# Performance work log

Hardware: AMD Instinct MI355X
Metric: run time of the kernel (lower is better)

The kernel has to match this reference:

```python
import jax, jax.numpy as jnp
import numpy as np

B, T, N, SD, D, HYP, EMB = 128, 256, 8, 200, 64, 64, 32

def _ln(x, g, b, eps=1e-5):
    mu = jnp.mean(x, -1, keepdims=True)
    v = jnp.mean((x - mu) ** 2, -1, keepdims=True)
    return (x - mu) * jax.lax.rsqrt(v + eps) * g + b

def setup_inputs():
    key = jax.random.key(0)
    ks = iter(jax.random.split(key, 64))
    def p(shape, scale=0.05):
        return (jax.random.normal(next(ks), shape) * scale).astype(jnp.float32)
    n, sd, d, hyp, emb = N, SD, D, HYP, EMB
    return dict(
        qvals=p((B, T, n), 1.0), states=p((B, T, sd), 1.0), hidden_state=p((B, T, n, d), 1.0),
        enc_w1=p((sd, d)), enc_b1=p((d,)), enc_w2=p((d, d)), enc_b2=p((d,)),
        wq=p((d, d)), bq=p((d,)), wk=p((d, d)), bk=p((d,)), wv=p((d, d)), bv=p((d,)),
        wo=p((d, d)), bo=p((d,)),
        ln1_g=jnp.ones((d,), jnp.float32), ln1_b=jnp.zeros((d,), jnp.float32),
        ffn_w1=p((d, d)), ffn_b1=p((d,)), ffn_w2=p((d, d)), ffn_b2=p((d,)),
        ln2_g=jnp.ones((d,), jnp.float32), ln2_b=jnp.zeros((d,), jnp.float32),
        fc2ni_w=p((n, d, n - 1)), fc2ni_b=p((n, n - 1)),
        norm_g=jnp.ones((n - 1,), jnp.float32), norm_b=jnp.zeros((n - 1,), jnp.float32),
        w1a=p((2 * d, hyp)), b1a=p((hyp,)), w1b=p((hyp, n * emb)), b1b=p((n * emb,)),
        hb1w=p((2 * d, emb)), hb1b=p((emb,)),
        w2a=p((2 * d, hyp)), b2a=p((hyp,)), w2b=p((hyp, emb)), b2b=p((emb,)),
        hb2w1=p((2 * d, emb)), hb2b1=p((emb,)), hb2w2=p((emb, 1)), hb2b2=p((1,)))

def reference(qvals, states, hidden_state, enc_w1, enc_b1, enc_w2, enc_b2,
              wq, bq, wk, bk, wv, bv, wo, bo, ln1_g, ln1_b,
              ffn_w1, ffn_b1, ffn_w2, ffn_b2, ln2_g, ln2_b,
              fc2ni_w, fc2ni_b, norm_g, norm_b,
              w1a, b1a, w1b, b1b, hb1w, hb1b,
              w2a, b2a, w2b, b2b, hb2w1, hb2b1, hb2w2, hb2b2):
    sg = jax.lax.stop_gradient
    b, t, n = qvals.shape
    bt = b * t
    d = hidden_state.shape[-1]
    emb = hb1w.shape[1]
    # Encoder_s: relu(fc1) then tanh(fc2(e)+e)
    s = states.reshape(bt, -1)
    e = jax.nn.relu(s @ enc_w1 + enc_b1)
    enc = jnp.tanh(e @ enc_w2 + enc_b2 + e)                       # (bt, 64)
    # concat detached agent hiddens with detached state embedding -> (bt, n+1, 64)
    h = jnp.concatenate([sg(hidden_state.reshape(bt, n, d)), sg(enc)[:, None, :]], axis=1)
    # transformer block (single-head self-attention + FFN, post-LN)
    q = h @ wq + bq; k = h @ wk + bk; v = h @ wv + bv
    att = jax.nn.softmax(jnp.einsum('bid,bjd->bij', q, k) / jnp.sqrt(jnp.float32(d)), axis=-1)
    h2 = _ln(h + (att @ v) @ wo + bo, ln1_g, ln1_b)
    h3 = _ln(h2 + jax.nn.relu(h2 @ ffn_w1 + ffn_b1) @ ffn_w2 + ffn_b2, ln2_g, ln2_b)
    h_trans = h3[:, :n]                                           # (bt, n, 64)
    ens = jnp.concatenate([enc, sg(h_trans).mean(1)], axis=-1)    # (bt, 128)
    # per-agent fc2_Ni -> LayerNorm -> sigmoid, vectorized over agents
    ni = jnp.einsum('xnd,nde->xne', h_trans, fc2ni_w) + fc2ni_b   # (bt, n, n-1)
    ni = jax.nn.sigmoid(_ln(ni, norm_g, norm_b))
    # insert 1.0 at the diagonal (agent i keeps its own q with weight 1)
    rows = jnp.arange(n)[:, None]; cols = jnp.arange(n)[None, :]
    gidx = jnp.clip(cols - (cols > rows).astype(jnp.int32), 0, n - 2)  # (n, n)
    gathered = jnp.take_along_axis(ni, jnp.broadcast_to(gidx, (bt, n, n)), axis=-1)
    nfull = jnp.where(cols == rows, jnp.float32(1.0), gathered)   # (bt, n, n)
    N_nn = nfull.reshape(b, t, n, n)
    q_ni = (qvals[:, :, None, :] * N_nn).sum(-1).reshape(bt, 1, n)
    # hypernetwork mixing (QMIX)
    ens_d = sg(ens)
    w1 = jnp.abs(jax.nn.relu(ens_d @ w1a + b1a) @ w1b + b1b).reshape(bt, n, emb)
    b1 = (ens_d @ hb1w + hb1b).reshape(bt, 1, emb)
    w2 = jnp.abs(jax.nn.relu(ens @ w2a + b2a) @ w2b + b2b).reshape(bt, emb, 1)
    b2 = (jax.nn.relu(ens @ hb2w1 + hb2b1) @ hb2w2 + hb2b2).reshape(bt, 1, 1)
    hidden = jax.nn.elu(q_ni @ w1 + b1)
    y = (hidden @ w2 + b2).reshape(b, t, 1)
    eye_mask = jnp.broadcast_to(jnp.eye(n, dtype=bool), (b, t, n, n))
    return y, N_nn, eye_mask
```

## Files before the change

kernel.cpp:

```cpp
#include <hip/hip_runtime.h>
#include <hip/hip_bf16.h>

typedef __bf16 bf16x8 __attribute__((ext_vector_type(8)));
typedef __bf16 bf16x4 __attribute__((ext_vector_type(4)));
typedef float f32x4 __attribute__((ext_vector_type(4)));

#define ROWSG 32768
#define RB 8
#define HPAD 72
#define NN_OFF ((size_t)ROWSG)
#define EYE_OFF ((size_t)ROWSG + (size_t)ROWSG*64)

#define OFF_EW1   0
#define OFF_EW2   14336
#define OFF_WQ    18432
#define OFF_WK    22528
#define OFF_WV    26624
#define OFF_WO    30720
#define OFF_F1    34816
#define OFF_F2    38912
#define OFF_W1A   43008
#define OFF_W1B   51200
#define OFF_HB1W  67584
#define OFF_W2A   71680
#define OFF_W2B   79872
#define OFF_HB2W1 81920
#define WS_TOTAL  86016
#define OFF_M     86016
#define WS_TOTAL2 90112

__device__ __align__(16) __bf16 g_ws[WS_TOTAL2];
__device__ float g_v[64];

#define MFMA16(a,b,c) __builtin_amdgcn_mfma_f32_16x16x32_bf16(a,b,c,0,0,0)

struct TP { const float* src[14]; };

__global__ __launch_bounds__(256) void wtrans(TP tp) {
    const int gid = blockIdx.x * 256 + threadIdx.x;
    if (gid >= WS_TOTAL) return;
    const int OFFS[14] = {OFF_EW1, OFF_EW2, OFF_WQ, OFF_WK, OFF_WV, OFF_WO, OFF_F1,
                          OFF_F2, OFF_W1A, OFF_W1B, OFF_HB1W, OFF_W2A, OFF_W2B, OFF_HB2W1};
    const int KPS[14]  = {224, 64, 64, 64, 64, 64, 64, 64, 128, 64, 128, 128, 64, 128};
    const int KRS[14]  = {200, 64, 64, 64, 64, 64, 64, 64, 128, 64, 128, 128, 64, 128};
    const int NS[14]   = {64, 64, 64, 64, 64, 64, 64, 64, 64, 256, 32, 64, 32, 32};
    int m = 0;
#pragma unroll
    for (int i = 1; i < 14; ++i) if (gid >= OFFS[i]) m = i;
    const int loc = gid - OFFS[m];
    const int Kp = KPS[m];
    const int n = loc / Kp;
    const int k = loc - n * Kp;
    float v = 0.f;
    if (k < KRS[m]) v = tp.src[m][(size_t)k * NS[m] + n];
    g_ws[gid] = (__bf16)v;
}

struct PP { const float *wq, *wk, *bq; };

__global__ __launch_bounds__(256) void wprep(PP pp) {
    const int t = threadIdx.x;
#pragma unroll 1
    for (int q = 0; q < 16; ++q) {
        const int idx = q * 256 + t;
        const int f = idx >> 6, e = idx & 63;
        float s = 0.f;
        for (int n = 0; n < 64; ++n) s += pp.wq[e * 64 + n] * pp.wk[f * 64 + n];
        g_ws[OFF_M + f * 64 + e] = (__bf16)(s * 0.125f);
    }
    if (t < 64) {
        float s = 0.f;
        for (int n = 0; n < 64; ++n) s += pp.wk[t * 64 + n] * pp.bq[n];
        g_v[t] = s * 0.125f;
    }
}

struct MainP {
    const float *qvals, *states, *hid, *eb1, *eb2, *bq, *bk, *bv, *bo,
        *l1g, *l1b, *fb1, *fb2, *l2g, *l2b, *niw, *nib, *ng, *nb,
        *b1a, *b1b, *hb1b, *b2a, *b2b, *hb2b1, *hw2, *hb2b2;
    float* out;
};

__device__ __forceinline__ void proj_ln_tile(const __bf16* A, const __bf16* WT,
                                             const float* bias, const float* g, const float* bb,
                                             __bf16* H, int mt, int quad, int l15) {
    f32x4 acc0 = {0,0,0,0}, acc1 = {0,0,0,0}, acc2 = {0,0,0,0}, acc3 = {0,0,0,0};
#pragma unroll
    for (int ks = 0; ks < 2; ++ks) {
        const int kk = ks * 32 + quad * 8;
        const bf16x8 af = *(const bf16x8*)(A + (mt * 16 + l15) * HPAD + kk);
        acc0 = MFMA16(af, *(const bf16x8*)(WT + (size_t)(0 * 16 + l15) * 64 + kk), acc0);
        acc1 = MFMA16(af, *(const bf16x8*)(WT + (size_t)(1 * 16 + l15) * 64 + kk), acc1);
        acc2 = MFMA16(af, *(const bf16x8*)(WT + (size_t)(2 * 16 + l15) * 64 + kk), acc2);
        acc3 = MFMA16(af, *(const bf16x8*)(WT + (size_t)(3 * 16 + l15) * 64 + kk), acc3);
    }
    float v[4][4], g4[4], b4[4];
#pragma unroll
    for (int nt = 0; nt < 4; ++nt) {
        const int col = nt * 16 + l15;
        const float bo = bias[col];
        g4[nt] = g[col]; b4[nt] = bb[col];
        const f32x4 a = (nt == 0) ? acc0 : (nt == 1) ? acc1 : (nt == 2) ? acc2 : acc3;
#pragma unroll
        for (int r = 0; r < 4; ++r)
            v[nt][r] = a[r] + bo + (float)H[(mt * 16 + quad * 4 + r) * HPAD + col];
    }
#pragma unroll
    for (int r = 0; r < 4; ++r) {
        float s  = v[0][r] + v[1][r] + v[2][r] + v[3][r];
        float s2 = v[0][r]*v[0][r] + v[1][r]*v[1][r] + v[2][r]*v[2][r] + v[3][r]*v[3][r];
#pragma unroll
        for (int off = 1; off < 16; off <<= 1) {
            s  += __shfl_xor(s,  off, 64);
            s2 += __shfl_xor(s2, off, 64);
        }
        const float mu  = s * 0.015625f;
        const float var = s2 * 0.015625f - mu * mu;
        const float rs  = rsqrtf(var + 1e-5f);
#pragma unroll
        for (int nt = 0; nt < 4; ++nt)
            H[(mt * 16 + quad * 4 + r) * HPAD + nt * 16 + l15] =
                (__bf16)((v[nt][r] - mu) * rs * g4[nt] + b4[nt]);
    }
}

template<int ACT>
__device__ __forceinline__ void proj_tile(const __bf16* A, const __bf16* WT, const float* bias,
                                          __bf16* D, int mt, int quad, int l15) {
    const int base = (mt * 16 + l15) * HPAD;
    const bf16x8 a0 = *(const bf16x8*)(A + base + quad * 8);
    const bf16x8 a1 = *(const bf16x8*)(A + base + 32 + quad * 8);
    f32x4 acc[4] = {{0,0,0,0},{0,0,0,0},{0,0,0,0},{0,0,0,0}};
#pragma unroll
    for (int nt = 0; nt < 4; ++nt) {
        acc[nt] = MFMA16(a0, *(const bf16x8*)(WT + (size_t)(nt * 16 + l15) * 64 + quad * 8), acc[nt]);
        acc[nt] = MFMA16(a1, *(const bf16x8*)(WT + (size_t)(nt * 16 + l15) * 64 + 32 + quad * 8), acc[nt]);
    }
#pragma unroll
    for (int nt = 0; nt < 4; ++nt) {
        const float bv = bias[nt * 16 + l15];
#pragma unroll
        for (int r = 0; r < 4; ++r) {
            float val = acc[nt][r] + bv;
            if (ACT == 1) val = fmaxf(val, 0.f);
            D[(mt * 16 + quad * 4 + r) * HPAD + nt * 16 + l15] = (__bf16)val;
        }
    }
}

__global__ __launch_bounds__(256) void mixer_main(MainP p) {
    __shared__ __align__(16) __bf16 Hb[80 * HPAD];
    __shared__ __align__(16) __bf16 Qb[80 * HPAD];
    __shared__ __align__(16) __bf16 EbU[16 * HPAD];
    __shared__ __align__(16) __bf16 Tb2[16 * HPAD];
    __shared__ __align__(16) __bf16 ensB[16 * 136];
    __shared__ __align__(16) char   uniB[3072];
    __shared__ float sQv[64];
    __shared__ float qniL[64];
    __shared__ float vhS[80];
    __shared__ __align__(16) __bf16 W1bS[8 * 256];

    float* attU = (float*)uniB;
    float* B1f  = (float*)uniB;
    float* W2f  = (float*)(uniB + 1024);
    float* T3f  = (float*)(uniB + 2048);
    float* sNi  = (float*)W1bS;
    __bf16* Sb  = W1bS;

    const int blk = blockIdx.x;
    const int bt0 = blk * RB;
    const int t = threadIdx.x;
    const int w = t >> 6, lane = t & 63, quad = lane >> 4, l15 = lane & 15;
    const __bf16* ws = g_ws;

#pragma unroll
    for (int it = 0; it < 4; ++it) {
        const int u = it * 256 + t;
        const int x = u >> 7, rem = u & 127, n = rem >> 4, d4 = (rem & 15) * 4;
        const float4 v4 = *(const float4*)(p.hid + ((size_t)(bt0 + x) * 512 + n * 64 + d4));
        bf16x4 o; o[0] = (__bf16)v4.x; o[1] = (__bf16)v4.y; o[2] = (__bf16)v4.z; o[3] = (__bf16)v4.w;
        *(bf16x4*)(Hb + (x * 9 + n) * HPAD + d4) = o;
    }
#pragma unroll
    for (int it = 0; it < 2; ++it) {
        const int u = it * 256 + t;
        if (u < 400) {
            const int xr = u / 50, c4 = u - xr * 50;
            const float4 v4 = *(const float4*)(p.states + (size_t)(bt0 + xr) * 200 + c4 * 4);
            bf16x4 o; o[0] = (__bf16)v4.x; o[1] = (__bf16)v4.y; o[2] = (__bf16)v4.z; o[3] = (__bf16)v4.w;
            *(bf16x4*)(Sb + xr * 224 + c4 * 4) = o;
        }
    }
    if (t < 192) { const int xr = t / 24, c = t - xr * 24; Sb[xr * 224 + 200 + c] = (__bf16)0.0f; }
    if (t < 64) sQv[t] = p.qvals[(size_t)(bt0 + (t >> 3)) * 8 + (t & 7)];
    __syncthreads();

    float e4[4];
    {
        const int n0 = w * 16;
        const int srow = (l15 < 8) ? l15 : 7;
        f32x4 acc = {0, 0, 0, 0};
        for (int ks = 0; ks < 7; ++ks) {
            const int kk = ks * 32 + quad * 8;
            const bf16x8 af = *(const bf16x8*)(Sb + srow * 224 + kk);
            const bf16x8 bf = *(const bf16x8*)(ws + OFF_EW1 + (size_t)(n0 + l15) * 224 + kk);
            acc = MFMA16(af, bf, acc);
        }
        const float b1 = p.eb1[n0 + l15];
#pragma unroll
        for (int r = 0; r < 4; ++r) {
            const float ev = fmaxf(acc[r] + b1, 0.f);
            e4[r] = ev;
            EbU[(quad * 4 + r) * HPAD + n0 + l15] = (__bf16)ev;
        }
    }
    __syncthreads();

    {
        const int n0 = w * 16;
        f32x4 acc = {0, 0, 0, 0};
#pragma unroll
        for (int ks = 0; ks < 2; ++ks) {
            const int kk = ks * 32 + quad * 8;
            const bf16x8 af = *(const bf16x8*)(EbU + l15 * HPAD + kk);
            const bf16x8 bf = *(const bf16x8*)(ws + OFF_EW2 + (size_t)(n0 + l15) * 64 + kk);
            acc = MFMA16(af, bf, acc);
        }
        const float b2 = p.eb2[n0 + l15];
#pragma unroll
        for (int r = 0; r < 4; ++r) {
            const int xr = quad * 4 + r;
            if (xr < RB) {
                const float ev = tanhf(acc[r] + e4[r] + b2);
                Hb[(xr * 9 + 8) * HPAD + n0 + l15] = (__bf16)ev;
                ensB[xr * 136 + n0 + l15] = (__bf16)ev;
            }
        }
    }
    __syncthreads();

    for (int it = 0; it < 5; ++it) {
        const int j = w + 4 * it;
        const int mt = j >> 2, nt = j & 3;
        f32x4 acc = {0, 0, 0, 0};
#pragma unroll
        for (int ks = 0; ks < 2; ++ks) {
            const int kk = ks * 32 + quad * 8;
            const bf16x8 af = *(const bf16x8*)(Hb + (mt * 16 + l15) * HPAD + kk);
            const bf16x8 bf = *(const bf16x8*)(ws + OFF_M + (size_t)(nt * 16 + l15) * 64 + kk);
            acc = MFMA16(af, bf, acc);
        }
#pragma unroll
        for (int r = 0; r < 4; ++r)
            Qb[(mt * 16 + quad * 4 + r) * HPAD + nt * 16 + l15] = (__bf16)acc[r];
    }
    if (t < 72) {
        float s = 0.f;
#pragma unroll
        for (int c8 = 0; c8 < 8; ++c8) {
            const bf16x8 hv = *(const bf16x8*)(Hb + t * HPAD + c8 * 8);
#pragma unroll
            for (int jj = 0; jj < 8; ++jj) s += (float)hv[jj] * g_v[c8 * 8 + jj];
        }
        vhS[t] = s;
    }
    __syncthreads();

    for (int xi = 0; xi < 2; ++xi) {
        const int x = w * 2 + xi;
        const int arow = (x * 9 + l15) * HPAD;
        f32x4 acc = {0, 0, 0, 0};
#pragma unroll
        for (int ks = 0; ks < 2; ++ks) {
            const int kk = ks * 32 + quad * 8;
            acc = MFMA16(*(const bf16x8*)(Qb + arow + kk), *(const bf16x8*)(Hb + arow + kk), acc);
        }
        const float vh = (l15 < 9) ? vhS[x * 9 + l15] : 0.f;
#pragma unroll
        for (int r = 0; r < 4; ++r) {
            const int i = quad * 4 + r;
            float s = (l15 < 9) ? (acc[r] + vh) : -3.0e38f;
            float m = s;
#pragma unroll
            for (int off = 1; off < 16; off <<= 1) m = fmaxf(m, __shfl_xor(m, off, 64));
            float e = (l15 < 9) ? __expf(s - m) : 0.f;
            float sum = e;
#pragma unroll
            for (int off = 1; off < 16; off <<= 1) sum += __shfl_xor(sum, off, 64);
            if (i < 9 && l15 < 9) attU[x * 81 + i * 9 + l15] = e / sum;
        }
        float vreg[9];
#pragma unroll
        for (int jj = 0; jj < 9; ++jj) vreg[jj] = (float)Hb[(x * 9 + jj) * HPAD + lane];
#pragma unroll
        for (int i = 0; i < 9; ++i) {
            float a = 0.f;
#pragma unroll
            for (int jj = 0; jj < 9; ++jj) a += attU[x * 81 + i * 9 + jj] * vreg[jj];
            Qb[(x * 9 + i) * HPAD + lane] = (__bf16)a;
        }
    }
    __syncthreads();

    for (int mti = 0; mti < 2; ++mti) {
        const int mt = w + 4 * mti;
        if (mt >= 5) continue;
        proj_tile<0>(Qb, ws + OFF_WV, p.bv, Qb, mt, quad, l15);
        proj_ln_tile(Qb, ws + OFF_WO, p.bo, p.l1g, p.l1b, Hb, mt, quad, l15);
        proj_tile<1>(Hb, ws + OFF_F1, p.fb1, Qb, mt, quad, l15);
        proj_ln_tile(Qb, ws + OFF_F2, p.fb2, p.l2g, p.l2b, Hb, mt, quad, l15);
    }
    __syncthreads();

#pragma unroll
    for (int it = 0; it < 2; ++it) {
        const int id = it * 256 + t;
        const int x = id >> 6, col = id & 63;
        float s = 0.f;
#pragma unroll
        for (int i = 0; i < 8; ++i) s += (float)Hb[(x * 9 + i) * HPAD + col];
        ensB[x * 136 + 64 + col] = (__bf16)(s * 0.125f);
    }
    {
        const int pr = t >> 2, q4 = t & 3;
        const int x = pr >> 3, n = pr & 7;
        float acc[7] = {0.f, 0.f, 0.f, 0.f, 0.f, 0.f, 0.f};
        const float* wni = p.niw + n * 448;
        for (int dd = 0; dd < 16; ++dd) {
            const int d = q4 * 16 + dd;
            const float hv = (float)Hb[(x * 9 + n) * HPAD + d];
#pragma unroll
            for (int e = 0; e < 7; ++e) acc[e] += hv * wni[d * 7 + e];
        }
#pragma unroll
        for (int e = 0; e < 7; ++e) {
            acc[e] += __shfl_xor(acc[e], 1, 64);
            acc[e] += __shfl_xor(acc[e], 2, 64);
        }
        if (q4 == 0) {
            float s = 0.f;
#pragma unroll
            for (int e = 0; e < 7; ++e) { acc[e] += p.nib[n * 7 + e]; s += acc[e]; }
            const float mu = s * (1.f / 7.f);
            float s2 = 0.f;
#pragma unroll
            for (int e = 0; e < 7; ++e) { const float d0 = acc[e] - mu; s2 += d0 * d0; }
            const float rs = rsqrtf(s2 * (1.f / 7.f) + 1e-5f);
#pragma unroll
            for (int e = 0; e < 7; ++e) {
                const float vv = (acc[e] - mu) * rs * p.ng[e] + p.nb[e];
                sNi[x * 64 + n * 8 + e] = 1.f / (1.f + __expf(-vv));
            }
        }
    }
    __syncthreads();

#pragma unroll
    for (int it = 0; it < 2; ++it) {
        const int id = it * 256 + t;
        const int x = id >> 6, rem = id & 63, i = rem >> 3, jj = rem & 7;
        const float nf = (i == jj) ? 1.f : sNi[x * 64 + i * 8 + (jj - (jj > i ? 1 : 0))];
        p.out[NN_OFF + (size_t)(bt0 + x) * 64 + rem] = nf;
        p.out[EYE_OFF + (size_t)(bt0 + x) * 64 + rem] = (i == jj) ? 1.f : 0.f;
    }
    {
        const int pr = t >> 2, q4 = t & 3;
        const int x = pr >> 3, i = pr & 7;
        float s = 0.f;
#pragma unroll
        for (int jo = 0; jo < 2; ++jo) {
            const int j = q4 * 2 + jo;
            const float nf = (j == i) ? 1.f : sNi[x * 64 + i * 8 + (j - (j > i ? 1 : 0))];
            s += sQv[x * 8 + j] * nf;
        }
        s += __shfl_xor(s, 1, 64);
        s += __shfl_xor(s, 2, 64);
        if (q4 == 0) qniL[x * 8 + i] = s;
    }
    {
        const int n0 = w * 16;
#pragma unroll
        for (int m2 = 0; m2 < 2; ++m2) {
            const __bf16* wt = ws + (m2 == 0 ? OFF_W1A : OFF_W2A);
            const float* bias = m2 == 0 ? p.b1a : p.b2a;
            __bf16* dst = m2 == 0 ? EbU : Tb2;
            f32x4 acc = {0, 0, 0, 0};
#pragma unroll
            for (int ks = 0; ks < 4; ++ks) {
                const int kk = ks * 32 + quad * 8;
                const bf16x8 af = *(const bf16x8*)(ensB + l15 * 136 + kk);
                const bf16x8 bf = *(const bf16x8*)(wt + (size_t)(n0 + l15) * 128 + kk);
                acc = MFMA16(af, bf, acc);
            }
            const float bb = bias[n0 + l15];
#pragma unroll
            for (int r = 0; r < 4; ++r)
                dst[(quad * 4 + r) * HPAD + n0 + l15] = (__bf16)fmaxf(acc[r] + bb, 0.f);
        }
    }
    __syncthreads();

    for (int it = 0; it < 6; ++it) {
        const int j = w + 4 * it;
        if (j >= 22) continue;
        int mode, n0, Kp, ksteps, aStride;
        const __bf16 *A, *WT; const float* bias;
        if (j < 16)      { mode = 0; n0 = j * 16;        A = EbU;  aStride = HPAD; WT = ws + OFF_W1B;   bias = p.b1b;  Kp = 64;  ksteps = 2; }
        else if (j < 18) { mode = 1; n0 = (j - 16) * 16; A = ensB; aStride = 136;  WT = ws + OFF_HB1W;  bias = p.hb1b; Kp = 128; ksteps = 4; }
        else if (j < 20) { mode = 2; n0 = (j - 18) * 16; A = Tb2;  aStride = HPAD; WT = ws + OFF_W2B;   bias = p.b2b;  Kp = 64;  ksteps = 2; }
        else             { mode = 3; n0 = (j - 20) * 16; A = ensB; aStride = 136;  WT = ws + OFF_HB2W1; bias = p.hb2b1;Kp = 128; ksteps = 4; }
        f32x4 acc = {0, 0, 0, 0};
        for (int ks = 0; ks < ksteps; ++ks) {
            const int kk = ks * 32 + quad * 8;
            const bf16x8 af = *(const bf16x8*)(A + l15 * aStride + kk);
            const bf16x8 bf = *(const bf16x8*)(WT + (size_t)(n0 + l15) * Kp + kk);
            acc = MFMA16(af, bf, acc);
        }
        const float bb = bias[n0 + l15];
#pragma unroll
        for (int r = 0; r < 4; ++r) {
            const int xr = quad * 4 + r;
            if (xr < RB) {
                const float val = acc[r] + bb;
                if (mode == 0)      W1bS[xr * 256 + n0 + l15] = (__bf16)fabsf(val);
                else if (mode == 1) B1f[xr * 32 + n0 + l15] = val;
                else if (mode == 2) W2f[xr * 32 + n0 + l15] = fabsf(val);
                else                T3f[xr * 32 + n0 + l15] = fmaxf(val, 0.f);
            }
        }
    }
    __syncthreads();

    if (t < 128) {
        const int x = t >> 4, sub = t & 15;
        float pp = 0.f, pb = 0.f;
#pragma unroll
        for (int h2i = 0; h2i < 2; ++h2i) {
            const int e = sub + h2i * 16;
            float a = B1f[x * 32 + e];
#pragma unroll
            for (int i = 0; i < 8; ++i) a += qniL[x * 8 + i] * (float)W1bS[x * 256 + i * 32 + e];
            const float hid = a > 0.f ? a : (__expf(a) - 1.f);
            pp += hid * W2f[x * 32 + e];
            pb += T3f[x * 32 + e] * p.hw2[e];
        }
#pragma unroll
        for (int off = 1; off < 16; off <<= 1) {
            pp += __shfl_xor(pp, off, 64);
            pb += __shfl_xor(pb, off, 64);
        }
        if (sub == 0) p.out[bt0 + x] = pp + pb + p.hb2b2[0];
    }
}

extern "C" void kernel_launch(void* const* d_in, const int* in_sizes, int n_in,
                              void* d_out, int out_size, void* d_ws, size_t ws_size,
                              hipStream_t stream) {
    TP tp;
    tp.src[0]  = (const float*)d_in[3];
    tp.src[1]  = (const float*)d_in[5];
    tp.src[2]  = (const float*)d_in[7];
    tp.src[3]  = (const float*)d_in[9];
    tp.src[4]  = (const float*)d_in[11];
    tp.src[5]  = (const float*)d_in[13];
    tp.src[6]  = (const float*)d_in[17];
    tp.src[7]  = (const float*)d_in[19];
    tp.src[8]  = (const float*)d_in[27];
    tp.src[9]  = (const float*)d_in[29];
    tp.src[10] = (const float*)d_in[31];
    tp.src[11] = (const float*)d_in[33];
    tp.src[12] = (const float*)d_in[35];
    tp.src[13] = (const float*)d_in[37];
    wtrans<<<(WS_TOTAL + 255) / 256, 256, 0, stream>>>(tp);

    PP pqk;
    pqk.wq = (const float*)d_in[7];
    pqk.wk = (const float*)d_in[9];
    pqk.bq = (const float*)d_in[8];
    wprep<<<1, 256, 0, stream>>>(pqk);

    MainP p;
    p.qvals = (const float*)d_in[0];
    p.states = (const float*)d_in[1];
    p.hid = (const float*)d_in[2];
    p.eb1 = (const float*)d_in[4];
    p.eb2 = (const float*)d_in[6];
    p.bq = (const float*)d_in[8];
    p.bk = (const float*)d_in[10];
    p.bv = (const float*)d_in[12];
    p.bo = (const float*)d_in[14];
    p.l1g = (const float*)d_in[15];
    p.l1b = (const float*)d_in[16];
    p.fb1 = (const float*)d_in[18];
    p.fb2 = (const float*)d_in[20];
    p.l2g = (const float*)d_in[21];
    p.l2b = (const float*)d_in[22];
    p.niw = (const float*)d_in[23];
    p.nib = (const float*)d_in[24];
    p.ng = (const float*)d_in[25];
    p.nb = (const float*)d_in[26];
    p.b1a = (const float*)d_in[28];
    p.b1b = (const float*)d_in[30];
    p.hb1b = (const float*)d_in[32];
    p.b2a = (const float*)d_in[34];
    p.b2b = (const float*)d_in[36];
    p.hb2b1 = (const float*)d_in[38];
    p.hw2 = (const float*)d_in[39];
    p.hb2b2 = (const float*)d_in[40];
    p.out = (float*)d_out;

    mixer_main<<<ROWSG / RB, 256, 0, stream>>>(p);
}
```

Measured before the change: 439.2 us.

## Restructure mixer into single-wave blocks of two rows without barriers

The main kernel now runs one 64-thread wavefront per block handling two batch-time rows instead of 256 threads handling eight. All __syncthreads barriers go away and shared memory shrinks to a dynamic 12.5KB layout, so more blocks can be resident. Each wave computes all output column tiles itself, with stores masked to the valid rows. The cost is that MFMA tiles are mostly padding (2 or 9 of 16 rows used), so much more matrix work and weight reloading happens per useful row. The weight-prep kernel is also spread across 17 blocks instead of one serial block.

```diff
diff --git a/kernel.cpp b/kernel.cpp
--- a/kernel.cpp
+++ b/kernel.cpp
@@ -6,7 +6,6 @@
 typedef float f32x4 __attribute__((ext_vector_type(4)));
 
 #define ROWSG 32768
-#define RB 8
 #define HPAD 72
 #define NN_OFF ((size_t)ROWSG)
 #define EYE_OFF ((size_t)ROWSG + (size_t)ROWSG*64)
@@ -34,6 +33,23 @@
 
 #define MFMA16(a,b,c) __builtin_amdgcn_mfma_f32_16x16x32_bf16(a,b,c,0,0,0)
 
+#define L_H    0
+#define L_W    2592
+#define L_SB   5184
+#define L_ENS  6080
+#define L_T1   6624
+#define L_T2   6912
+#define L_W1S  7200
+#define L_ATT  8224
+#define L_SNI  8872
+#define L_VH   9384
+#define L_QV   9464
+#define L_QNI  9528
+#define L_B1F  9592
+#define L_W2F  9848
+#define L_T3F  10104
+#define L_TOTAL 12544
+
 struct TP { const float* src[14]; };
 
 __global__ __launch_bounds__(256) void wtrans(TP tp) {
@@ -59,16 +75,14 @@
 struct PP { const float *wq, *wk, *bq; };
 
 __global__ __launch_bounds__(256) void wprep(PP pp) {
-    const int t = threadIdx.x;
-#pragma unroll 1
-    for (int q = 0; q < 16; ++q) {
-        const int idx = q * 256 + t;
+    const int b = blockIdx.x, t = threadIdx.x;
+    if (b < 16) {
+        const int idx = b * 256 + t;
         const int f = idx >> 6, e = idx & 63;
         float s = 0.f;
         for (int n = 0; n < 64; ++n) s += pp.wq[e * 64 + n] * pp.wk[f * 64 + n];
         g_ws[OFF_M + f * 64 + e] = (__bf16)(s * 0.125f);
-    }
-    if (t < 64) {
+    } else if (t < 64) {
         float s = 0.f;
         for (int n = 0; n < 64; ++n) s += pp.wk[t * 64 + n] * pp.bq[n];
         g_v[t] = s * 0.125f;
@@ -82,18 +96,40 @@
     float* out;
 };
 
-__device__ __forceinline__ void proj_ln_tile(const __bf16* A, const __bf16* WT,
-                                             const float* bias, const float* g, const float* bb,
-                                             __bf16* H, int mt, int quad, int l15) {
-    f32x4 acc0 = {0,0,0,0}, acc1 = {0,0,0,0}, acc2 = {0,0,0,0}, acc3 = {0,0,0,0};
+template<bool RELU>
+__device__ __forceinline__ void projT(const __bf16* A, const __bf16* WT, const float* bias,
+                                      __bf16* D, int quad, int l15) {
+    const bf16x8 a0 = *(const bf16x8*)(A + l15 * HPAD + quad * 8);
+    const bf16x8 a1 = *(const bf16x8*)(A + l15 * HPAD + 32 + quad * 8);
+    f32x4 acc[4] = {{0,0,0,0},{0,0,0,0},{0,0,0,0},{0,0,0,0}};
+#pragma unroll
+    for (int nt = 0; nt < 4; ++nt) {
+        acc[nt] = MFMA16(a0, *(const bf16x8*)(WT + (size_t)(nt * 16 + l15) * 64 + quad * 8), acc[nt]);
+        acc[nt] = MFMA16(a1, *(const bf16x8*)(WT + (size_t)(nt * 16 + l15) * 64 + 32 + quad * 8), acc[nt]);
+    }
+#pragma unroll
+    for (int nt = 0; nt < 4; ++nt) {
+        const float bv = bias[nt * 16 + l15];
+#pragma unroll
+        for (int r = 0; r < 4; ++r) {
+            float val = acc[nt][r] + bv;
+            if (RELU) val = fmaxf(val, 0.f);
+            if (quad * 4 + r < 9) D[(quad * 4 + r) * HPAD + nt * 16 + l15] = (__bf16)val;
+        }
+    }
+}
+
+__device__ __forceinline__ void projLN(const __bf16* A, const __bf16* WT, const float* bias,
+                                       const float* g, const float* bb, __bf16* Hd,
+                                       int quad, int l15) {
+    f32x4 acc[4] = {{0,0,0,0},{0,0,0,0},{0,0,0,0},{0,0,0,0}};
 #pragma unroll
     for (int ks = 0; ks < 2; ++ks) {
         const int kk = ks * 32 + quad * 8;
-        const bf16x8 af = *(const bf16x8*)(A + (mt * 16 + l15) * HPAD + kk);
-        acc0 = MFMA16(af, *(const bf16x8*)(WT + (size_t)(0 * 16 + l15) * 64 + kk), acc0);
-        acc1 = MFMA16(af, *(const bf16x8*)(WT + (size_t)(1 * 16 + l15) * 64 + kk), acc1);
-        acc2 = MFMA16(af, *(const bf16x8*)(WT + (size_t)(2 * 16 + l15) * 64 + kk), acc2);
-        acc3 = MFMA16(af, *(const bf16x8*)(WT + (size_t)(3 * 16 + l15) * 64 + kk), acc3);
+        const bf16x8 af = *(const bf16x8*)(A + l15 * HPAD + kk);
+#pragma unroll
+        for (int nt = 0; nt < 4; ++nt)
+            acc[nt] = MFMA16(af, *(const bf16x8*)(WT + (size_t)(nt * 16 + l15) * 64 + kk), acc[nt]);
     }
     float v[4][4], g4[4], b4[4];
 #pragma unroll
@@ -101,10 +137,9 @@
         const int col = nt * 16 + l15;
         const float bo = bias[col];
         g4[nt] = g[col]; b4[nt] = bb[col];
-        const f32x4 a = (nt == 0) ? acc0 : (nt == 1) ? acc1 : (nt == 2) ? acc2 : acc3;
 #pragma unroll
         for (int r = 0; r < 4; ++r)
-            v[nt][r] = a[r] + bo + (float)H[(mt * 16 + quad * 4 + r) * HPAD + col];
+            v[nt][r] = acc[nt][r] + bo + (float)Hd[(quad * 4 + r) * HPAD + col];
     }
 #pragma unroll
     for (int r = 0; r < 4; ++r) {
@@ -120,161 +155,140 @@
         const float rs  = rsqrtf(var + 1e-5f);
 #pragma unroll
         for (int nt = 0; nt < 4; ++nt)
-            H[(mt * 16 + quad * 4 + r) * HPAD + nt * 16 + l15] =
-                (__bf16)((v[nt][r] - mu) * rs * g4[nt] + b4[nt]);
+            if (quad * 4 + r < 9)
+                Hd[(quad * 4 + r) * HPAD + nt * 16 + l15] =
+                    (__bf16)((v[nt][r] - mu) * rs * g4[nt] + b4[nt]);
     }
 }
 
-template<int ACT>
-__device__ __forceinline__ void proj_tile(const __bf16* A, const __bf16* WT, const float* bias,
-                                          __bf16* D, int mt, int quad, int l15) {
-    const int base = (mt * 16 + l15) * HPAD;
-    const bf16x8 a0 = *(const bf16x8*)(A + base + quad * 8);
-    const bf16x8 a1 = *(const bf16x8*)(A + base + 32 + quad * 8);
-    f32x4 acc[4] = {{0,0,0,0},{0,0,0,0},{0,0,0,0},{0,0,0,0}};
-#pragma unroll
-    for (int nt = 0; nt < 4; ++nt) {
-        acc[nt] = MFMA16(a0, *(const bf16x8*)(WT + (size_t)(nt * 16 + l15) * 64 + quad * 8), acc[nt]);
-        acc[nt] = MFMA16(a1, *(const bf16x8*)(WT + (size_t)(nt * 16 + l15) * 64 + 32 + quad * 8), acc[nt]);
-    }
-#pragma unroll
-    for (int nt = 0; nt < 4; ++nt) {
-        const float bv = bias[nt * 16 + l15];
-#pragma unroll
-        for (int r = 0; r < 4; ++r) {
-            float val = acc[nt][r] + bv;
-            if (ACT == 1) val = fmaxf(val, 0.f);
-            D[(mt * 16 + quad * 4 + r) * HPAD + nt * 16 + l15] = (__bf16)val;
-        }
-    }
-}
-
-__global__ __launch_bounds__(256) void mixer_main(MainP p) {
-    __shared__ __align__(16) __bf16 Hb[80 * HPAD];
-    __shared__ __align__(16) __bf16 Qb[80 * HPAD];
-    __shared__ __align__(16) __bf16 EbU[16 * HPAD];
-    __shared__ __align__(16) __bf16 Tb2[16 * HPAD];
-    __shared__ __align__(16) __bf16 ensB[16 * 136];
-    __shared__ __align__(16) char   uniB[3072];
-    __shared__ float sQv[64];
-    __shared__ float qniL[64];
-    __shared__ float vhS[80];
-    __shared__ __align__(16) __bf16 W1bS[8 * 256];
-
-    float* attU = (float*)uniB;
-    float* B1f  = (float*)uniB;
-    float* W2f  = (float*)(uniB + 1024);
-    float* T3f  = (float*)(uniB + 2048);
-    float* sNi  = (float*)W1bS;
-    __bf16* Sb  = W1bS;
-
-    const int blk = blockIdx.x;
-    const int bt0 = blk * RB;
-    const int t = threadIdx.x;
-    const int w = t >> 6, lane = t & 63, quad = lane >> 4, l15 = lane & 15;
+__global__ __launch_bounds__(64, 4) void mixer_main(MainP p) {
+    extern __shared__ __align__(16) char smraw[];
+    __bf16* H    = (__bf16*)(smraw + L_H);
+    __bf16* W    = (__bf16*)(smraw + L_W);
+    __bf16* Sb   = (__bf16*)(smraw + L_SB);
+    __bf16* ensB = (__bf16*)(smraw + L_ENS);
+    __bf16* T1   = (__bf16*)(smraw + L_T1);
+    __bf16* T2   = (__bf16*)(smraw + L_T2);
+    __bf16* w1S  = (__bf16*)(smraw + L_W1S);
+    float* attU  = (float*)(smraw + L_ATT);
+    float* sNi   = (float*)(smraw + L_SNI);
+    float* vhS   = (float*)(smraw + L_VH);
+    float* sQv   = (float*)(smraw + L_QV);
+    float* qniL  = (float*)(smraw + L_QNI);
+    float* B1f   = (float*)(smraw + L_B1F);
+    float* W2f   = (float*)(smraw + L_W2F);
+    float* T3f   = (float*)(smraw + L_T3F);
+
+    const int bt0 = blockIdx.x * 2;
+    const int lane = threadIdx.x;
+    const int quad = lane >> 4, l15 = lane & 15;
     const __bf16* ws = g_ws;
 
 #pragma unroll
     for (int it = 0; it < 4; ++it) {
-        const int u = it * 256 + t;
+        const int u = it * 64 + lane;
         const int x = u >> 7, rem = u & 127, n = rem >> 4, d4 = (rem & 15) * 4;
         const float4 v4 = *(const float4*)(p.hid + ((size_t)(bt0 + x) * 512 + n * 64 + d4));
         bf16x4 o; o[0] = (__bf16)v4.x; o[1] = (__bf16)v4.y; o[2] = (__bf16)v4.z; o[3] = (__bf16)v4.w;
-        *(bf16x4*)(Hb + (x * 9 + n) * HPAD + d4) = o;
+        *(bf16x4*)(H + (x * 9 + n) * HPAD + d4) = o;
     }
 #pragma unroll
     for (int it = 0; it < 2; ++it) {
-        const int u = it * 256 + t;
-        if (u < 400) {
+        const int u = it * 64 + lane;
+        if (u < 100) {
             const int xr = u / 50, c4 = u - xr * 50;
             const float4 v4 = *(const float4*)(p.states + (size_t)(bt0 + xr) * 200 + c4 * 4);
             bf16x4 o; o[0] = (__bf16)v4.x; o[1] = (__bf16)v4.y; o[2] = (__bf16)v4.z; o[3] = (__bf16)v4.w;
             *(bf16x4*)(Sb + xr * 224 + c4 * 4) = o;
         }
     }
-    if (t < 192) { const int xr = t / 24, c = t - xr * 24; Sb[xr * 224 + 200 + c] = (__bf16)0.0f; }
-    if (t < 64) sQv[t] = p.qvals[(size_t)(bt0 + (t >> 3)) * 8 + (t & 7)];
-    __syncthreads();
-
-    float e4[4];
+    if (lane < 48) { const int xr = lane / 24, c = lane - xr * 24; Sb[xr * 224 + 200 + c] = (__bf16)0.0f; }
+    if (lane < 16) sQv[lane] = p.qvals[(size_t)bt0 * 8 + lane];
+
+    float e_reg[4][4];
     {
-        const int n0 = w * 16;
-        const int srow = (l15 < 8) ? l15 : 7;
+        f32x4 acc[4] = {{0,0,0,0},{0,0,0,0},{0,0,0,0},{0,0,0,0}};
+        for (int ks = 0; ks < 7; ++ks) {
+            const int kk = ks * 32 + quad * 8;
+            const bf16x8 af = *(const bf16x8*)(Sb + l15 * 224 + kk);
+#pragma unroll
+            for (int nt = 0; nt < 4; ++nt)
+                acc[nt] = MFMA16(af, *(const bf16x8*)(ws + OFF_EW1 + (size_t)(nt * 16 + l15) * 224 + kk), acc[nt]);
+        }
+#pragma unroll
+        for (int nt = 0; nt < 4; ++nt) {
+            const float b1 = p.eb1[nt * 16 + l15];
+#pragma unroll
+            for (int r = 0; r < 4; ++r) {
+                const float ev = fmaxf(acc[nt][r] + b1, 0.f);
+                e_reg[nt][r] = ev;
+                if (quad * 4 + r < 2) W[(quad * 4 + r) * HPAD + nt * 16 + l15] = (__bf16)ev;
+            }
+        }
+    }
+
+    {
+        f32x4 acc[4] = {{0,0,0,0},{0,0,0,0},{0,0,0,0},{0,0,0,0}};
+#pragma unroll
+        for (int ks = 0; ks < 2; ++ks) {
+            const int kk = ks * 32 + quad * 8;
+            const bf16x8 af = *(const bf16x8*)(W + l15 * HPAD + kk);
+#pragma unroll
+            for (int nt = 0; nt < 4; ++nt)
+                acc[nt] = MFMA16(af, *(const bf16x8*)(ws + OFF_EW2 + (size_t)(nt * 16 + l15) * 64 + kk), acc[nt]);
+        }
+#pragma unroll
+        for (int nt = 0; nt < 4; ++nt) {
+            const float b2 = p.eb2[nt * 16 + l15];
+#pragma unroll
+            for (int r = 0; r < 4; ++r) {
+                const int xr = quad * 4 + r;
+                if (xr < 2) {
+                    const float ev = tanhf(acc[nt][r] + e_reg[nt][r] + b2);
+                    H[(xr * 9 + 8) * HPAD + nt * 16 + l15] = (__bf16)ev;
+                    ensB[xr * 136 + nt * 16 + l15] = (__bf16)ev;
+                }
+            }
+        }
+    }
+
+    for (int x = 0; x < 2; ++x) {
+        const __bf16* A = H + x * 9 * HPAD;
+        f32x4 acc[4] = {{0,0,0,0},{0,0,0,0},{0,0,0,0},{0,0,0,0}};
+#pragma unroll
+        for (int ks = 0; ks < 2; ++ks) {
+            const int kk = ks * 32 + quad * 8;
+            const bf16x8 af = *(const bf16x8*)(A + l15 * HPAD + kk);
+#pragma unroll
+            for (int nt = 0; nt < 4; ++nt)
+                acc[nt] = MFMA16(af, *(const bf16x8*)(ws + OFF_M + (size_t)(nt * 16 + l15) * 64 + kk), acc[nt]);
+        }
+#pragma unroll
+        for (int nt = 0; nt < 4; ++nt)
+#pragma unroll
+            for (int r = 0; r < 4; ++r)
+                if (quad * 4 + r < 9)
+                    W[(x * 9 + quad * 4 + r) * HPAD + nt * 16 + l15] = (__bf16)acc[nt][r];
+    }
+    if (lane < 18) {
+        float s = 0.f;
+#pragma unroll
+        for (int c8 = 0; c8 < 8; ++c8) {
+            const bf16x8 hv = *(const bf16x8*)(H + lane * HPAD + c8 * 8);
+#pragma unroll
+            for (int jj = 0; jj < 8; ++jj) s += (float)hv[jj] * g_v[c8 * 8 + jj];
+        }
+        vhS[lane] = s;
+    }
+
+    for (int x = 0; x < 2; ++x) {
+        const int base = x * 9 * HPAD;
         f32x4 acc = {0, 0, 0, 0};
-        for (int ks = 0; ks < 7; ++ks) {
-            const int kk = ks * 32 + quad * 8;
-            const bf16x8 af = *(const bf16x8*)(Sb + srow * 224 + kk);
-            const bf16x8 bf = *(const bf16x8*)(ws + OFF_EW1 + (size_t)(n0 + l15) * 224 + kk);
-            acc = MFMA16(af, bf, acc);
-        }
-        const float b1 = p.eb1[n0 + l15];
-#pragma unroll
-        for (int r = 0; r < 4; ++r) {
-            const float ev = fmaxf(acc[r] + b1, 0.f);
-            e4[r] = ev;
-            EbU[(quad * 4 + r) * HPAD + n0 + l15] = (__bf16)ev;
-        }
-    }
-    __syncthreads();
-
-    {
-        const int n0 = w * 16;
-        f32x4 acc = {0, 0, 0, 0};
 #pragma unroll
         for (int ks = 0; ks < 2; ++ks) {
             const int kk = ks * 32 + quad * 8;
-            const bf16x8 af = *(const bf16x8*)(EbU + l15 * HPAD + kk);
-            const bf16x8 bf = *(const bf16x8*)(ws + OFF_EW2 + (size_t)(n0 + l15) * 64 + kk);
-            acc = MFMA16(af, bf, acc);
-        }
-        const float b2 = p.eb2[n0 + l15];
-#pragma unroll
-        for (int r = 0; r < 4; ++r) {
-            const int xr = quad * 4 + r;
-            if (xr < RB) {
-                const float ev = tanhf(acc[r] + e4[r] + b2);
-                Hb[(xr * 9 + 8) * HPAD + n0 + l15] = (__bf16)ev;
-                ensB[xr * 136 + n0 + l15] = (__bf16)ev;
-            }
-        }
-    }
-    __syncthreads();
-
-    for (int it = 0; it < 5; ++it) {
-        const int j = w + 4 * it;
-        const int mt = j >> 2, nt = j & 3;
-        f32x4 acc = {0, 0, 0, 0};
-#pragma unroll
-        for (int ks = 0; ks < 2; ++ks) {
-            const int kk = ks * 32 + quad * 8;
-            const bf16x8 af = *(const bf16x8*)(Hb + (mt * 16 + l15) * HPAD + kk);
-            const bf16x8 bf = *(const bf16x8*)(ws + OFF_M + (size_t)(nt * 16 + l15) * 64 + kk);
-            acc = MFMA16(af, bf, acc);
-        }
-#pragma unroll
-        for (int r = 0; r < 4; ++r)
-            Qb[(mt * 16 + quad * 4 + r) * HPAD + nt * 16 + l15] = (__bf16)acc[r];
-    }
-    if (t < 72) {
-        float s = 0.f;
-#pragma unroll
-        for (int c8 = 0; c8 < 8; ++c8) {
-            const bf16x8 hv = *(const bf16x8*)(Hb + t * HPAD + c8 * 8);
-#pragma unroll
-            for (int jj = 0; jj < 8; ++jj) s += (float)hv[jj] * g_v[c8 * 8 + jj];
-        }
-        vhS[t] = s;
-    }
-    __syncthreads();
-
-    for (int xi = 0; xi < 2; ++xi) {
-        const int x = w * 2 + xi;
-        const int arow = (x * 9 + l15) * HPAD;
-        f32x4 acc = {0, 0, 0, 0};
-#pragma unroll
-        for (int ks = 0; ks < 2; ++ks) {
-            const int kk = ks * 32 + quad * 8;
-            acc = MFMA16(*(const bf16x8*)(Qb + arow + kk), *(const bf16x8*)(Hb + arow + kk), acc);
+            acc = MFMA16(*(const bf16x8*)(W + base + l15 * HPAD + kk),
+                         *(const bf16x8*)(H + base + l15 * HPAD + kk), acc);
         }
         const float vh = (l15 < 9) ? vhS[x * 9 + l15] : 0.f;
 #pragma unroll
@@ -292,44 +306,40 @@
         }
         float vreg[9];
 #pragma unroll
-        for (int jj = 0; jj < 9; ++jj) vreg[jj] = (float)Hb[(x * 9 + jj) * HPAD + lane];
+        for (int jj = 0; jj < 9; ++jj) vreg[jj] = (float)H[base + jj * HPAD + lane];
 #pragma unroll
         for (int i = 0; i < 9; ++i) {
             float a = 0.f;
 #pragma unroll
             for (int jj = 0; jj < 9; ++jj) a += attU[x * 81 + i * 9 + jj] * vreg[jj];
-            Qb[(x * 9 + i) * HPAD + lane] = (__bf16)a;
-        }
-    }
-    __syncthreads();
-
-    for (int mti = 0; mti < 2; ++mti) {
-        const int mt = w + 4 * mti;
-        if (mt >= 5) continue;
-        proj_tile<0>(Qb, ws + OFF_WV, p.bv, Qb, mt, quad, l15);
-        proj_ln_tile(Qb, ws + OFF_WO, p.bo, p.l1g, p.l1b, Hb, mt, quad, l15);
-        proj_tile<1>(Hb, ws + OFF_F1, p.fb1, Qb, mt, quad, l15);
-        proj_ln_tile(Qb, ws + OFF_F2, p.fb2, p.l2g, p.l2b, Hb, mt, quad, l15);
-    }
-    __syncthreads();
-
-#pragma unroll
-    for (int it = 0; it < 2; ++it) {
-        const int id = it * 256 + t;
-        const int x = id >> 6, col = id & 63;
+            W[base + i * HPAD + lane] = (__bf16)a;
+        }
+    }
+
+    for (int x = 0; x < 2; ++x) {
+        __bf16* Wb = W + x * 9 * HPAD;
+        __bf16* Hb = H + x * 9 * HPAD;
+        projT<false>(Wb, ws + OFF_WV, p.bv, Wb, quad, l15);
+        projLN(Wb, ws + OFF_WO, p.bo, p.l1g, p.l1b, Hb, quad, l15);
+        projT<true>(Hb, ws + OFF_F1, p.fb1, Wb, quad, l15);
+        projLN(Wb, ws + OFF_F2, p.fb2, p.l2g, p.l2b, Hb, quad, l15);
+    }
+
+    for (int x = 0; x < 2; ++x) {
         float s = 0.f;
 #pragma unroll
-        for (int i = 0; i < 8; ++i) s += (float)Hb[(x * 9 + i) * HPAD + col];
-        ensB[x * 136 + 64 + col] = (__bf16)(s * 0.125f);
-    }
+        for (int i = 0; i < 8; ++i) s += (float)H[(x * 9 + i) * HPAD + lane];
+        ensB[x * 136 + 64 + lane] = (__bf16)(s * 0.125f);
+    }
+
     {
-        const int pr = t >> 2, q4 = t & 3;
+        const int pr = lane >> 2, q4 = lane & 3;
         const int x = pr >> 3, n = pr & 7;
         float acc[7] = {0.f, 0.f, 0.f, 0.f, 0.f, 0.f, 0.f};
         const float* wni = p.niw + n * 448;
         for (int dd = 0; dd < 16; ++dd) {
             const int d = q4 * 16 + dd;
-            const float hv = (float)Hb[(x * 9 + n) * HPAD + d];
+            const float hv = (float)H[(x * 9 + n) * HPAD + d];
 #pragma unroll
             for (int e = 0; e < 7; ++e) acc[e] += hv * wni[d * 7 + e];
         }
@@ -354,18 +364,17 @@
             }
         }
     }
-    __syncthreads();
 
 #pragma unroll
     for (int it = 0; it < 2; ++it) {
-        const int id = it * 256 + t;
+        const int id = it * 64 + lane;
         const int x = id >> 6, rem = id & 63, i = rem >> 3, jj = rem & 7;
         const float nf = (i == jj) ? 1.f : sNi[x * 64 + i * 8 + (jj - (jj > i ? 1 : 0))];
         p.out[NN_OFF + (size_t)(bt0 + x) * 64 + rem] = nf;
         p.out[EYE_OFF + (size_t)(bt0 + x) * 64 + rem] = (i == jj) ? 1.f : 0.f;
     }
     {
-        const int pr = t >> 2, q4 = t & 3;
+        const int pr = lane >> 2, q4 = lane & 3;
         const int x = pr >> 3, i = pr & 7;
         float s = 0.f;
 #pragma unroll
@@ -378,79 +387,85 @@
         s += __shfl_xor(s, 2, 64);
         if (q4 == 0) qniL[x * 8 + i] = s;
     }
-    {
-        const int n0 = w * 16;
-#pragma unroll
-        for (int m2 = 0; m2 < 2; ++m2) {
-            const __bf16* wt = ws + (m2 == 0 ? OFF_W1A : OFF_W2A);
-            const float* bias = m2 == 0 ? p.b1a : p.b2a;
-            __bf16* dst = m2 == 0 ? EbU : Tb2;
-            f32x4 acc = {0, 0, 0, 0};
-#pragma unroll
-            for (int ks = 0; ks < 4; ++ks) {
-                const int kk = ks * 32 + quad * 8;
-                const bf16x8 af = *(const bf16x8*)(ensB + l15 * 136 + kk);
-                const bf16x8 bf = *(const bf16x8*)(wt + (size_t)(n0 + l15) * 128 + kk);
-                acc = MFMA16(af, bf, acc);
-            }
-            const float bb = bias[n0 + l15];
+
+#pragma unroll
+    for (int m2 = 0; m2 < 2; ++m2) {
+        const __bf16* wt = ws + (m2 == 0 ? OFF_W1A : OFF_W2A);
+        const float* bias = m2 == 0 ? p.b1a : p.b2a;
+        __bf16* dst = m2 == 0 ? T1 : T2;
+        f32x4 acc[4] = {{0,0,0,0},{0,0,0,0},{0,0,0,0},{0,0,0,0}};
+#pragma unroll
+        for (int ks = 0; ks < 4; ++ks) {
+            const int kk = ks * 32 + quad * 8;
+            const bf16x8 af = *(const bf16x8*)(ensB + l15 * 136 + kk);
+#pragma unroll
+            for (int nt = 0; nt < 4; ++nt)
+                acc[nt] = MFMA16(af, *(const bf16x8*)(wt + (size_t)(nt * 16 + l15) * 128 + kk), acc[nt]);
+        }
+#pragma unroll
+        for (int nt = 0; nt < 4; ++nt) {
+            const float bb = bias[nt * 16 + l15];
 #pragma unroll
             for (int r = 0; r < 4; ++r)
-                dst[(quad * 4 + r) * HPAD + n0 + l15] = (__bf16)fmaxf(acc[r] + bb, 0.f);
-        }
-    }
-    __syncthreads();
-
-    for (int it = 0; it < 6; ++it) {
-        const int j = w + 4 * it;
-        if (j >= 22) continue;
-        int mode, n0, Kp, ksteps, aStride;
-        const __bf16 *A, *WT; const float* bias;
-        if (j < 16)      { mode = 0; n0 = j * 16;        A = EbU;  aStride = HPAD; WT = ws + OFF_W1B;   bias = p.b1b;  Kp = 64;  ksteps = 2; }
-        else if (j < 18) { mode = 1; n0 = (j - 16) * 16; A = ensB; aStride = 136;  WT = ws + OFF_HB1W;  bias = p.hb1b; Kp = 128; ksteps = 4; }
-        else if (j < 20) { mode = 2; n0 = (j - 18) * 16; A = Tb2;  aStride = HPAD; WT = ws + OFF_W2B;   bias = p.b2b;  Kp = 64;  ksteps = 2; }
-        else             { mode = 3; n0 = (j - 20) * 16; A = ensB; aStride = 136;  WT = ws + OFF_HB2W1; bias = p.hb2b1;Kp = 128; ksteps = 4; }
+                if (quad * 4 + r < 2)
+                    dst[(quad * 4 + r) * HPAD + nt * 16 + l15] = (__bf16)fmaxf(acc[nt][r] + bb, 0.f);
+        }
+    }
+
+    for (int nt16 = 0; nt16 < 16; ++nt16) {
         f32x4 acc = {0, 0, 0, 0};
-        for (int ks = 0; ks < ksteps; ++ks) {
-            const int kk = ks * 32 + quad * 8;
-            const bf16x8 af = *(const bf16x8*)(A + l15 * aStride + kk);
-            const bf16x8 bf = *(const bf16x8*)(WT + (size_t)(n0 + l15) * Kp + kk);
-            acc = MFMA16(af, bf, acc);
-        }
-        const float bb = bias[n0 + l15];
+#pragma unroll
+        for (int ks = 0; ks < 2; ++ks) {
+            const int kk = ks * 32 + quad * 8;
+            acc = MFMA16(*(const bf16x8*)(T1 + l15 * HPAD + kk),
+                         *(const bf16x8*)(ws + OFF_W1B + (size_t)(nt16 * 16 + l15) * 64 + kk), acc);
+        }
+        const float bb = p.b1b[nt16 * 16 + l15];
+#pragma unroll
+        for (int r = 0; r < 4; ++r)
+            if (quad * 4 + r < 2)
+                w1S[(quad * 4 + r) * 256 + nt16 * 16 + l15] = (__bf16)fabsf(acc[r] + bb);
+    }
+#pragma unroll
+    for (int nt = 0; nt < 2; ++nt) {
+        f32x4 accB = {0,0,0,0}, accT = {0,0,0,0}, accW = {0,0,0,0};
+#pragma unroll
+        for (int ks = 0; ks < 4; ++ks) {
+            const int kk = ks * 32 + quad * 8;
+            const bf16x8 af = *(const bf16x8*)(ensB + l15 * 136 + kk);
+            accB = MFMA16(af, *(const bf16x8*)(ws + OFF_HB1W  + (size_t)(nt * 16 + l15) * 128 + kk), accB);
+            accT = MFMA16(af, *(const bf16x8*)(ws + OFF_HB2W1 + (size_t)(nt * 16 + l15) * 128 + kk), accT);
+        }
+#pragma unroll
+        for (int ks = 0; ks < 2; ++ks) {
+            const int kk = ks * 32 + quad * 8;
+            accW = MFMA16(*(const bf16x8*)(T2 + l15 * HPAD + kk),
+                          *(const bf16x8*)(ws + OFF_W2B + (size_t)(nt * 16 + l15) * 64 + kk), accW);
+        }
+        const float bB = p.hb1b[nt * 16 + l15];
+        const float bT = p.hb2b1[nt * 16 + l15];
+        const float bW = p.b2b[nt * 16 + l15];
 #pragma unroll
         for (int r = 0; r < 4; ++r) {
             const int xr = quad * 4 + r;
-            if (xr < RB) {
-                const float val = acc[r] + bb;
-                if (mode == 0)      W1bS[xr * 256 + n0 + l15] = (__bf16)fabsf(val);
-                else if (mode == 1) B1f[xr * 32 + n0 + l15] = val;
-                else if (mode == 2) W2f[xr * 32 + n0 + l15] = fabsf(val);
-                else                T3f[xr * 32 + n0 + l15] = fmaxf(val, 0.f);
+            if (xr < 2) {
+                B1f[xr * 32 + nt * 16 + l15] = accB[r] + bB;
+                T3f[xr * 32 + nt * 16 + l15] = fmaxf(accT[r] + bT, 0.f);
+                W2f[xr * 32 + nt * 16 + l15] = fabsf(accW[r] + bW);
             }
         }
     }
-    __syncthreads();
-
-    if (t < 128) {
-        const int x = t >> 4, sub = t & 15;
-        float pp = 0.f, pb = 0.f;
-#pragma unroll
-        for (int h2i = 0; h2i < 2; ++h2i) {
-            const int e = sub + h2i * 16;
-            float a = B1f[x * 32 + e];
-#pragma unroll
-            for (int i = 0; i < 8; ++i) a += qniL[x * 8 + i] * (float)W1bS[x * 256 + i * 32 + e];
-            const float hid = a > 0.f ? a : (__expf(a) - 1.f);
-            pp += hid * W2f[x * 32 + e];
-            pb += T3f[x * 32 + e] * p.hw2[e];
-        }
-#pragma unroll
-        for (int off = 1; off < 16; off <<= 1) {
-            pp += __shfl_xor(pp, off, 64);
-            pb += __shfl_xor(pb, off, 64);
-        }
-        if (sub == 0) p.out[bt0 + x] = pp + pb + p.hb2b2[0];
+
+    {
+        const int x = lane >> 5, sub = lane & 31;
+        float a = B1f[x * 32 + sub];
+#pragma unroll
+        for (int i = 0; i < 8; ++i) a += qniL[x * 8 + i] * (float)w1S[x * 256 + i * 32 + sub];
+        const float hid = a > 0.f ? a : (__expf(a) - 1.f);
+        float red = hid * W2f[x * 32 + sub] + T3f[x * 32 + sub] * p.hw2[sub];
+#pragma unroll
+        for (int off = 1; off < 32; off <<= 1) red += __shfl_xor(red, off, 64);
+        if (sub == 0) p.out[bt0 + x] = red + p.hb2b2[0];
     }
 }
 
@@ -478,7 +493,7 @@
     pqk.wq = (const float*)d_in[7];
     pqk.wk = (const float*)d_in[9];
     pqk.bq = (const float*)d_in[8];
-    wprep<<<1, 256, 0, stream>>>(pqk);
+    wprep<<<17, 256, 0, stream>>>(pqk);
 
     MainP p;
     p.qvals = (const float*)d_in[0];
@@ -510,5 +525,5 @@
     p.hb2b2 = (const float*)d_in[40];
     p.out = (float*)d_out;
 
-    mixer_main<<<ROWSG / RB, 256, 0, stream>>>(p);
+    mixer_main<<<ROWSG / 2, 64, L_TOTAL, stream>>>(p);
 }
```

New measurement: 681.2 us. 55.1% more time.
